# Kernel optimization log

Hardware: AMD Instinct MI355X
Metric: run time of the kernel (lower is better)

Reference implementation:

```python
import jax, jax.numpy as jnp
import numpy as np

INPUT_DIM = 1024
HIDDEN_DIM = 64  # per-head dim
NUM_HEADS = 16
LN_EPS = 1e-5


def setup_inputs() -> dict:
    key = jax.random.key(0)
    ks = jax.random.split(key, 12)
    B, S, D = 2, 2048, INPUT_DIM
    HD = HIDDEN_DIM * NUM_HEADS
    s_in = 1.0 / np.sqrt(D)
    s_hd = 1.0 / np.sqrt(HD)
    return {
        "x": jax.random.normal(ks[0], (B, S, D), dtype=jnp.float32),
        "Wq": jax.random.normal(ks[1], (D, HD), dtype=jnp.float32) * s_in,
        "bq": jax.random.normal(ks[2], (HD,), dtype=jnp.float32) * 0.02,
        "Wk": jax.random.normal(ks[3], (D, HD), dtype=jnp.float32) * s_in,
        "bk": jax.random.normal(ks[4], (HD,), dtype=jnp.float32) * 0.02,
        "Wv": jax.random.normal(ks[5], (D, HD), dtype=jnp.float32) * s_in,
        "bv": jax.random.normal(ks[6], (HD,), dtype=jnp.float32) * 0.02,
        "Wo": jax.random.normal(ks[7], (HD, D), dtype=jnp.float32) * s_hd,
        "bo": jax.random.normal(ks[8], (D,), dtype=jnp.float32) * 0.02,
        "gamma": jnp.ones((D,), dtype=jnp.float32),
        "beta": jnp.zeros((D,), dtype=jnp.float32),
    }


def _layer_norm(y, gamma, beta):
    mu = jnp.mean(y, axis=-1, keepdims=True)
    var = jnp.mean(jnp.square(y - mu), axis=-1, keepdims=True)
    return (y - mu) * jax.lax.rsqrt(var + LN_EPS) * gamma + beta


def reference(x, Wq, bq, Wk, bk, Wv, bv, Wo, bo, gamma, beta):
    B, S, D = x.shape
    H, Hd = NUM_HEADS, HIDDEN_DIM
    # Faithful to the torch module: (B,S,H*Hd) -> reshape (B,H,S,Hd) WITHOUT transpose.
    Q = (x @ Wq + bq).reshape(B, H, S, Hd)
    K = (x @ Wk + bk).reshape(B, H, S, Hd)
    V = (x @ Wv + bv).reshape(B, H, S, Hd)
    scores = jnp.einsum("bhqd,bhkd->bhqk", Q, K) / jnp.sqrt(jnp.float32(Hd))
    attn = jax.nn.softmax(scores, axis=-1)  # dropout=0 -> identity
    ctx = jnp.einsum("bhqk,bhkd->bhqd", attn, V).reshape(B, S, H * Hd)
    out = _layer_norm(x + (ctx @ Wo + bo), gamma, beta)
    return jax.nn.gelu(out, approximate=False)
```

## Files before the change

kernel.cpp:

```cpp
#include <hip/hip_runtime.h>
#include <hip/hip_bf16.h>
#include <cstdint>
#include <cstddef>


#define SEQ   2048
#define DIM   1024
#define NHEAD 16
#define HDIM  64
#define ROWS  4096

#define QSCALE 0.1803368801111204f

typedef __attribute__((ext_vector_type(8))) __bf16 bf16x8;
typedef __attribute__((ext_vector_type(4))) float floatx4;
typedef __attribute__((ext_vector_type(8))) unsigned short ushortx8;

__device__ __forceinline__ unsigned short f2bf(float f) {
  unsigned int u = __float_as_uint(f);
  u += 0x7FFFu + ((u >> 16) & 1u);
  return (unsigned short)(u >> 16);
}

__device__ __forceinline__ unsigned int pk2bf(float a, float b) {
  float2 f; f.x = a; f.y = b;
  __hip_bfloat162 h = __float22bfloat162_rn(f);
  return *(unsigned int*)&h;
}

__device__ __forceinline__ void glds16(const unsigned short* g,
                                       unsigned short* l) {
  __builtin_amdgcn_global_load_lds(
      (const __attribute__((address_space(1))) void*)g,
      (__attribute__((address_space(3))) void*)l, 16, 0, 0);
}

__global__ __launch_bounds__(256) void cvt_bf16(const float* __restrict__ in,
                                                unsigned short* __restrict__ out,
                                                int n4) {
  int i = blockIdx.x * 256 + threadIdx.x;
  if (i >= n4) return;
  float4 v = ((const float4*)in)[i];
  ushort4 o;
  o.x = f2bf(v.x); o.y = f2bf(v.y); o.z = f2bf(v.z); o.w = f2bf(v.w);
  ((ushort4*)out)[i] = o;
}

__global__ __launch_bounds__(256) void transpose_w4(
    const float* __restrict__ Wq, const float* __restrict__ Wk,
    const float* __restrict__ Wv, const float* __restrict__ Wo,
    unsigned short* __restrict__ Wqkvt, unsigned short* __restrict__ Wot) {
  __shared__ float t[32][33];
  const int z = blockIdx.z;
  const float* in = (z == 0) ? Wq : (z == 1) ? Wk : (z == 2) ? Wv : Wo;
  unsigned short* out = (z < 3) ? Wqkvt + (size_t)z * DIM * DIM : Wot;
  const int bx = blockIdx.x * 32, by = blockIdx.y * 32;
  const int tx = threadIdx.x, ty = threadIdx.y;
#pragma unroll
  for (int i = ty; i < 32; i += 8)
    t[i][tx] = in[(size_t)(by + i) * DIM + bx + tx];
  __syncthreads();
#pragma unroll
  for (int i = ty; i < 32; i += 8)
    out[(size_t)(bx + i) * DIM + by + tx] = f2bf(t[tx][i]);
}

__global__ __launch_bounds__(256) void swizzle_kv(
    unsigned short* __restrict__ Kb,
    const unsigned short* __restrict__ Vb,
    unsigned short* __restrict__ Vs) {
  __shared__ unsigned short t[64 * 72];
  const int tile = blockIdx.x;
  const int bh   = blockIdx.y;
  const int isV  = blockIdx.z;
  const int tid  = threadIdx.x;
  const size_t base = (size_t)bh * (SEQ * HDIM) + (size_t)tile * 4096;
  const unsigned short* src = (isV ? Vb : Kb) + base;
#pragma unroll
  for (int p = 0; p < 2; ++p) {
    const int c = p * 256 + tid;
    *(ushortx8*)&t[(c >> 3) * 72 + (c & 7) * 8] = *(const ushortx8*)&src[c * 8];
  }
  __syncthreads();
  unsigned short* dst = (isV ? Vs : Kb) + base;
  const int lane = tid & 63, wave = tid >> 6;
  const int l16 = lane & 15, quad = lane >> 4;
  if (!isV) {
#pragma unroll
    for (int p = 0; p < 2; ++p) {
      const int f = wave * 2 + p;
      const int step = f >> 2, g = f & 3;
      *(ushortx8*)&dst[f * 512 + lane * 8] =
          *(const ushortx8*)&t[(g * 16 + l16) * 72 + step * 32 + quad * 8];
    }
  } else {
#pragma unroll
    for (int p = 0; p < 2; ++p) {
      const int f = wave * 2 + p;
      const int step = f >> 2, g = f & 3;
      ushortx8 v;
#pragma unroll
      for (int e = 0; e < 8; ++e)
        v[e] = t[(step * 32 + quad * 8 + e) * 72 + g * 16 + l16];
      *(ushortx8*)&dst[f * 512 + lane * 8] = v;
    }
  }
}

__global__ __launch_bounds__(256, 3) void gemm_qkv(
    const unsigned short* __restrict__ A,
    const unsigned short* __restrict__ Wt,
    const float* __restrict__ bq, const float* __restrict__ bk,
    const float* __restrict__ bv,
    unsigned short* __restrict__ Qb, unsigned short* __restrict__ Kb,
    unsigned short* __restrict__ Vb) {
  constexpr int K = DIM;
  __shared__ unsigned short As[128 * 64];
  __shared__ unsigned short Bs[128 * 64];
  const int tid  = threadIdx.x;
  const int lane = tid & 63, wave = tid >> 6;
  const int l16  = lane & 15, quad = lane >> 4;
  const int wm   = (wave & 1) * 64, wn = (wave >> 1) * 64;
  const int tm   = blockIdx.y * 128, tn = blockIdx.x * 128;
  const int grow = lane >> 3, gcol = (lane & 7) * 8;

  floatx4 acc[4][4] = {};

  for (int k0 = 0; k0 < K; k0 += 64) {
    __syncthreads();
#pragma unroll
    for (int p = 0; p < 4; ++p) {
      const int q = wave * 4 + p;
      const int row = q * 8 + grow;
      glds16(&A [(size_t)(tm + row) * K + k0 + gcol], &As[q * 512]);
      glds16(&Wt[(size_t)(tn + row) * K + k0 + gcol], &Bs[q * 512]);
    }
    __syncthreads();
#pragma unroll
    for (int step = 0; step < 2; ++step) {
      const int kk = step * 32 + quad * 8;
      bf16x8 af[4], bfr[4];
#pragma unroll
      for (int i = 0; i < 4; ++i)
        af[i] = *(const bf16x8*)&As[(wm + i * 16 + l16) * 64 + kk];
#pragma unroll
      for (int j = 0; j < 4; ++j)
        bfr[j] = *(const bf16x8*)&Bs[(wn + j * 16 + l16) * 64 + kk];
#pragma unroll
      for (int i = 0; i < 4; ++i)
#pragma unroll
        for (int j = 0; j < 4; ++j)
          acc[i][j] = __builtin_amdgcn_mfma_f32_16x16x32_bf16(af[i], bfr[j],
                                                              acc[i][j], 0, 0, 0);
    }
  }

#pragma unroll
  for (int j = 0; j < 4; ++j) {
    const int ng  = tn + wn + j * 16 + l16;
    const int seg = ng >> 10;
    const int col = ng & 1023;
    const float* bp    = (seg == 0) ? bq : (seg == 1) ? bk : bv;
    unsigned short* op = (seg == 0) ? Qb : (seg == 1) ? Kb : Vb;
    const float bias = bp[col];
    const float scl  = (seg == 0) ? QSCALE : 1.0f;
#pragma unroll
    for (int i = 0; i < 4; ++i) {
      const int m0 = tm + wm + i * 16 + quad * 4;
#pragma unroll
      for (int r = 0; r < 4; ++r)
        op[(size_t)(m0 + r) * DIM + col] = f2bf((acc[i][j][r] + bias) * scl);
    }
  }
}

__global__ __launch_bounds__(256) void gemm_o(
    const unsigned short* __restrict__ A,
    const unsigned short* __restrict__ Wt,
    const float* __restrict__ bo,
    float* __restrict__ Y) {
  constexpr int K = DIM;
  __shared__ unsigned short As[128 * 64];
  __shared__ unsigned short Bs[64 * 64];
  const int tid  = threadIdx.x;
  const int lane = tid & 63, wave = tid >> 6;
  const int l16  = lane & 15, quad = lane >> 4;
  const int wm   = wave * 32;
  const int tm   = blockIdx.y * 128, tn = blockIdx.x * 64;
  const int grow = lane >> 3, gcol = (lane & 7) * 8;

  floatx4 acc[2][4] = {};

  for (int k0 = 0; k0 < K; k0 += 64) {
    __syncthreads();
#pragma unroll
    for (int p = 0; p < 4; ++p) {
      const int q = wave * 4 + p;
      const int row = q * 8 + grow;
      glds16(&A[(size_t)(tm + row) * K + k0 + gcol], &As[q * 512]);
    }
#pragma unroll
    for (int p = 0; p < 2; ++p) {
      const int q = wave * 2 + p;
      const int row = q * 8 + grow;
      glds16(&Wt[(size_t)(tn + row) * K + k0 + gcol], &Bs[q * 512]);
    }
    __syncthreads();
#pragma unroll
    for (int step = 0; step < 2; ++step) {
      const int kk = step * 32 + quad * 8;
      bf16x8 af[2], bfr[4];
#pragma unroll
      for (int i = 0; i < 2; ++i)
        af[i] = *(const bf16x8*)&As[(wm + i * 16 + l16) * 64 + kk];
#pragma unroll
      for (int j = 0; j < 4; ++j)
        bfr[j] = *(const bf16x8*)&Bs[(j * 16 + l16) * 64 + kk];
#pragma unroll
      for (int i = 0; i < 2; ++i)
#pragma unroll
        for (int j = 0; j < 4; ++j)
          acc[i][j] = __builtin_amdgcn_mfma_f32_16x16x32_bf16(af[i], bfr[j],
                                                              acc[i][j], 0, 0, 0);
    }
  }

#pragma unroll
  for (int j = 0; j < 4; ++j) {
    const int n = tn + j * 16 + l16;
    const float bias = bo[n];
#pragma unroll
    for (int i = 0; i < 2; ++i) {
      const int m0 = tm + wm + i * 16 + quad * 4;
#pragma unroll
      for (int r = 0; r < 4; ++r)
        Y[(size_t)(m0 + r) * DIM + n] = acc[i][j][r] + bias;
    }
  }
}

__global__ __launch_bounds__(128) void attn_fwd(
    const unsigned short* __restrict__ Qb,
    const unsigned short* __restrict__ Ks,
    const unsigned short* __restrict__ Vs,
    unsigned short* __restrict__ Op0, unsigned short* __restrict__ Op1,
    float* __restrict__ l0, float* __restrict__ l1) {
  __shared__ unsigned short Pl[2][32 * 72];

  const int tid  = threadIdx.x;
  const int lane = tid & 63, wave = tid >> 6;
  const int l16  = lane & 15, quad = lane >> 4;
  const int id   = blockIdx.x;
  const int w    = id >> 3;
  const int head = (id & 7) * 4 + (w & 3);
  const int qt   = (w >> 2) & 31;
  const int half = w >> 7;
  const size_t slab = (size_t)head * SEQ * HDIM;
  const unsigned short* Q  = Qb + slab;
  const unsigned short* Kf = Ks + slab;
  const unsigned short* Vf = Vs + slab;
  const int q0 = qt * 64 + wave * 32;

  bf16x8 qf[2][2];
#pragma unroll
  for (int h = 0; h < 2; ++h) {
    qf[h][0] = *(const bf16x8*)&Q[(size_t)(q0 + h * 16 + l16) * HDIM + quad * 8];
    qf[h][1] = *(const bf16x8*)&Q[(size_t)(q0 + h * 16 + l16) * HDIM + 32 + quad * 8];
  }

  floatx4 o[2][4] = {};
  float lr[2] = {0.f, 0.f};

  for (int t = 0; t < 16; ++t) {
    const int tile = half * 16 + t;
    const unsigned short* kb = Kf + (size_t)tile * 4096;
    const unsigned short* vb = Vf + (size_t)tile * 4096;
    bf16x8 kf[2][4], vf[2][4];
#pragma unroll
    for (int step = 0; step < 2; ++step)
#pragma unroll
      for (int g = 0; g < 4; ++g) {
        kf[step][g] = *(const bf16x8*)&kb[(step * 4 + g) * 512 + lane * 8];
        vf[step][g] = *(const bf16x8*)&vb[(step * 4 + g) * 512 + lane * 8];
      }

    floatx4 s[2][4] = {};
#pragma unroll
    for (int step = 0; step < 2; ++step)
#pragma unroll
      for (int mt = 0; mt < 4; ++mt) {
        s[0][mt] = __builtin_amdgcn_mfma_f32_16x16x32_bf16(kf[step][mt], qf[0][step], s[0][mt], 0, 0, 0);
        s[1][mt] = __builtin_amdgcn_mfma_f32_16x16x32_bf16(kf[step][mt], qf[1][step], s[1][mt], 0, 0, 0);
      }

#pragma unroll
    for (int h = 0; h < 2; ++h) {
#pragma unroll
      for (int mt = 0; mt < 4; ++mt) {
        float p0 = __builtin_amdgcn_exp2f(s[h][mt][0]);
        float p1 = __builtin_amdgcn_exp2f(s[h][mt][1]);
        float p2 = __builtin_amdgcn_exp2f(s[h][mt][2]);
        float p3 = __builtin_amdgcn_exp2f(s[h][mt][3]);
        lr[h] += (p0 + p1) + (p2 + p3);
        uint2 pv;
        pv.x = pk2bf(p0, p1);
        pv.y = pk2bf(p2, p3);
        *(uint2*)&Pl[wave][(h * 16 + l16) * 72 + mt * 16 + quad * 4] = pv;
      }
    }
    __asm__ __volatile__("s_waitcnt lgkmcnt(0)" ::: "memory");

#pragma unroll
    for (int step = 0; step < 2; ++step) {
      const int kk = step * 32 + quad * 8;
      bf16x8 pf0 = *(const bf16x8*)&Pl[wave][(l16) * 72 + kk];
      bf16x8 pf1 = *(const bf16x8*)&Pl[wave][(16 + l16) * 72 + kk];
#pragma unroll
      for (int j = 0; j < 4; ++j) {
        o[0][j] = __builtin_amdgcn_mfma_f32_16x16x32_bf16(pf0, vf[step][j], o[0][j], 0, 0, 0);
        o[1][j] = __builtin_amdgcn_mfma_f32_16x16x32_bf16(pf1, vf[step][j], o[1][j], 0, 0, 0);
      }
    }
  }

#pragma unroll
  for (int h = 0; h < 2; ++h) {
    lr[h] += __shfl_xor(lr[h], 16, 64);
    lr[h] += __shfl_xor(lr[h], 32, 64);
  }
  unsigned short* Op = half ? Op1 : Op0;
  float*          lp = half ? l1 : l0;
#pragma unroll
  for (int h = 0; h < 2; ++h) {
    if (quad == 0)
      lp[head * SEQ + q0 + h * 16 + l16] = lr[h];
#pragma unroll
    for (int j = 0; j < 4; ++j)
#pragma unroll
      for (int r = 0; r < 4; ++r)
        Op[slab + (size_t)(q0 + h * 16 + quad * 4 + r) * HDIM + j * 16 + l16] =
            f2bf(o[h][j][r]);
  }
}

__global__ __launch_bounds__(256) void attn_merge(
    const unsigned short* __restrict__ Op0,
    const unsigned short* __restrict__ Op1,
    const float* __restrict__ l0, const float* __restrict__ l1,
    unsigned short* __restrict__ Cx) {
  const int i = blockIdx.x * 256 + threadIdx.x;
  const float inv = 1.0f / (l0[i >> 3] + l1[i >> 3]);
  ushortx8 a = *(const ushortx8*)&Op0[(size_t)i * 8];
  ushortx8 b = *(const ushortx8*)&Op1[(size_t)i * 8];
  ushortx8 o;
#pragma unroll
  for (int e = 0; e < 8; ++e) {
    const float fa = __uint_as_float((unsigned int)a[e] << 16);
    const float fb = __uint_as_float((unsigned int)b[e] << 16);
    o[e] = f2bf((fa + fb) * inv);
  }
  *(ushortx8*)&Cx[(size_t)i * 8] = o;
}

__global__ __launch_bounds__(256) void ln_gelu(
    const float* __restrict__ x, const float* __restrict__ y,
    const float* __restrict__ gamma, const float* __restrict__ beta,
    float* __restrict__ out) {
  const int row = blockIdx.x;
  const int tid = threadIdx.x;
  const float4 xv = ((const float4*)(x + (size_t)row * DIM))[tid];
  const float4 yv = ((const float4*)(y + (size_t)row * DIM))[tid];
  float4 s;
  s.x = xv.x + yv.x; s.y = xv.y + yv.y; s.z = xv.z + yv.z; s.w = xv.w + yv.w;
  float sum = (s.x + s.y) + (s.z + s.w);
  float sq  = (s.x * s.x + s.y * s.y) + (s.z * s.z + s.w * s.w);
#pragma unroll
  for (int off = 1; off < 64; off <<= 1) {
    sum += __shfl_xor(sum, off, 64);
    sq  += __shfl_xor(sq, off, 64);
  }
  __shared__ float red[8];
  const int wave = tid >> 6, lane = tid & 63;
  if (lane == 0) { red[wave] = sum; red[wave + 4] = sq; }
  __syncthreads();
  sum = red[0] + red[1] + red[2] + red[3];
  sq  = red[4] + red[5] + red[6] + red[7];
  const float mu   = sum * (1.0f / DIM);
  const float var  = sq * (1.0f / DIM) - mu * mu;
  const float rstd = rsqrtf(var + 1e-5f);
  const float4 gv = ((const float4*)gamma)[tid];
  const float4 bv = ((const float4*)beta)[tid];
  float4 ov;
  {
    const float v = (s.x - mu) * rstd * gv.x + bv.x;
    ov.x = 0.5f * v * (1.0f + erff(v * 0.70710678118654752f));
  }
  {
    const float v = (s.y - mu) * rstd * gv.y + bv.y;
    ov.y = 0.5f * v * (1.0f + erff(v * 0.70710678118654752f));
  }
  {
    const float v = (s.z - mu) * rstd * gv.z + bv.z;
    ov.z = 0.5f * v * (1.0f + erff(v * 0.70710678118654752f));
  }
  {
    const float v = (s.w - mu) * rstd * gv.w + bv.w;
    ov.w = 0.5f * v * (1.0f + erff(v * 0.70710678118654752f));
  }
  ((float4*)(out + (size_t)row * DIM))[tid] = ov;
}

extern "C" void kernel_launch(void* const* d_in, const int* in_sizes, int n_in,
                              void* d_out, int out_size, void* d_ws, size_t ws_size,
                              hipStream_t stream) {
  (void)in_sizes; (void)n_in; (void)out_size; (void)ws_size;
  const float* x     = (const float*)d_in[0];
  const float* Wq    = (const float*)d_in[1];
  const float* bq    = (const float*)d_in[2];
  const float* Wk    = (const float*)d_in[3];
  const float* bk    = (const float*)d_in[4];
  const float* Wv    = (const float*)d_in[5];
  const float* bv    = (const float*)d_in[6];
  const float* Wo    = (const float*)d_in[7];
  const float* bo    = (const float*)d_in[8];
  const float* gamma = (const float*)d_in[9];
  const float* beta  = (const float*)d_in[10];
  float* out = (float*)d_out;

  char* ws = (char*)d_ws;
  const size_t MB = 1u << 20;
  unsigned short* xb    = (unsigned short*)(ws);
  unsigned short* Op0   = (unsigned short*)(ws);
  unsigned short* Wqkvt = (unsigned short*)(ws + 8 * MB);
  float*          lp0   = (float*)(ws + 8 * MB);
  float*          lp1   = (float*)(ws + 8 * MB + 256 * 1024);
  unsigned short* Wot   = (unsigned short*)(ws + 14 * MB);
  unsigned short* Qb    = (unsigned short*)(ws + 16 * MB);
  unsigned short* Kb    = (unsigned short*)(ws + 24 * MB);
  unsigned short* Vs    = (unsigned short*)(ws + 32 * MB);
  unsigned short* Vb    = (unsigned short*)(ws + 40 * MB);
  unsigned short* Cx    = (unsigned short*)(ws + 40 * MB);
  float*          Y     = (float*)(ws + 48 * MB);
  unsigned short* Op1   = (unsigned short*)(ws + 48 * MB);

  cvt_bf16<<<(ROWS * DIM / 4 + 255) / 256, 256, 0, stream>>>(x, xb, ROWS * DIM / 4);
  transpose_w4<<<dim3(32, 32, 4), dim3(32, 8), 0, stream>>>(Wq, Wk, Wv, Wo, Wqkvt, Wot);

  gemm_qkv<<<dim3(24, 32), 256, 0, stream>>>(xb, Wqkvt, bq, bk, bv, Qb, Kb, Vb);
  swizzle_kv<<<dim3(SEQ / 64, 32, 2), 256, 0, stream>>>(Kb, Vb, Vs);
  attn_fwd<<<2048, 128, 0, stream>>>(Qb, Kb, Vs, Op0, Op1, lp0, lp1);
  attn_merge<<<(ROWS * DIM) / (8 * 256), 256, 0, stream>>>(Op0, Op1, lp0, lp1, Cx);
  gemm_o<<<dim3(16, 32), 256, 0, stream>>>(Cx, Wot, bo, Y);
  ln_gelu<<<ROWS, 256, 0, stream>>>(x, Y, gamma, beta, out);
}
```

Baseline: 220.4 us.

## Fuse split-K attention merge into attn_fwd via LDS and merge prep kernels

```diff
diff --git a/kernel.cpp b/kernel.cpp
--- a/kernel.cpp
+++ b/kernel.cpp
@@ -35,27 +35,31 @@
       (__attribute__((address_space(3))) void*)l, 16, 0, 0);
 }
 
-__global__ __launch_bounds__(256) void cvt_bf16(const float* __restrict__ in,
-                                                unsigned short* __restrict__ out,
-                                                int n4) {
-  int i = blockIdx.x * 256 + threadIdx.x;
-  if (i >= n4) return;
-  float4 v = ((const float4*)in)[i];
-  ushort4 o;
-  o.x = f2bf(v.x); o.y = f2bf(v.y); o.z = f2bf(v.z); o.w = f2bf(v.w);
-  ((ushort4*)out)[i] = o;
-}
-
-__global__ __launch_bounds__(256) void transpose_w4(
+__global__ __launch_bounds__(256) void prep_all(
+    const float* __restrict__ x,
     const float* __restrict__ Wq, const float* __restrict__ Wk,
     const float* __restrict__ Wv, const float* __restrict__ Wo,
+    unsigned short* __restrict__ xb,
     unsigned short* __restrict__ Wqkvt, unsigned short* __restrict__ Wot) {
   __shared__ float t[32][33];
   const int z = blockIdx.z;
+  const int tx = threadIdx.x, ty = threadIdx.y;
+  if (z == 4) {
+    const int bid = blockIdx.y * 32 + blockIdx.x;
+    const int tid = ty * 32 + tx;
+#pragma unroll
+    for (int p = 0; p < 4; ++p) {
+      const int i = bid * 1024 + p * 256 + tid;
+      float4 v = ((const float4*)x)[i];
+      ushort4 o;
+      o.x = f2bf(v.x); o.y = f2bf(v.y); o.z = f2bf(v.z); o.w = f2bf(v.w);
+      ((ushort4*)xb)[i] = o;
+    }
+    return;
+  }
   const float* in = (z == 0) ? Wq : (z == 1) ? Wk : (z == 2) ? Wv : Wo;
   unsigned short* out = (z < 3) ? Wqkvt + (size_t)z * DIM * DIM : Wot;
   const int bx = blockIdx.x * 32, by = blockIdx.y * 32;
-  const int tx = threadIdx.x, ty = threadIdx.y;
 #pragma unroll
   for (int i = ty; i < 32; i += 8)
     t[i][tx] = in[(size_t)(by + i) * DIM + bx + tx];
@@ -239,13 +243,12 @@
   }
 }
 
-__global__ __launch_bounds__(128) void attn_fwd(
+__global__ __launch_bounds__(256) void attn_fwd(
     const unsigned short* __restrict__ Qb,
     const unsigned short* __restrict__ Ks,
     const unsigned short* __restrict__ Vs,
-    unsigned short* __restrict__ Op0, unsigned short* __restrict__ Op1,
-    float* __restrict__ l0, float* __restrict__ l1) {
-  __shared__ unsigned short Pl[2][32 * 72];
+    unsigned short* __restrict__ ctx) {
+  __shared__ unsigned short Pl[4][32 * 72];
 
   const int tid  = threadIdx.x;
   const int lane = tid & 63, wave = tid >> 6;
@@ -253,13 +256,12 @@
   const int id   = blockIdx.x;
   const int w    = id >> 3;
   const int head = (id & 7) * 4 + (w & 3);
-  const int qt   = (w >> 2) & 31;
-  const int half = w >> 7;
+  const int qt   = w >> 2;
   const size_t slab = (size_t)head * SEQ * HDIM;
   const unsigned short* Q  = Qb + slab;
   const unsigned short* Kf = Ks + slab;
   const unsigned short* Vf = Vs + slab;
-  const int q0 = qt * 64 + wave * 32;
+  const int q0 = qt * 32;
 
   bf16x8 qf[2][2];
 #pragma unroll
@@ -271,8 +273,8 @@
   floatx4 o[2][4] = {};
   float lr[2] = {0.f, 0.f};
 
-  for (int t = 0; t < 16; ++t) {
-    const int tile = half * 16 + t;
+  for (int t = 0; t < 8; ++t) {
+    const int tile = wave * 8 + t;
     const unsigned short* kb = Kf + (size_t)tile * 4096;
     const unsigned short* vb = Vf + (size_t)tile * 4096;
     bf16x8 kf[2][4], vf[2][4];
@@ -328,38 +330,48 @@
     lr[h] += __shfl_xor(lr[h], 16, 64);
     lr[h] += __shfl_xor(lr[h], 32, 64);
   }
-  unsigned short* Op = half ? Op1 : Op0;
-  float*          lp = half ? l1 : l0;
-#pragma unroll
-  for (int h = 0; h < 2; ++h) {
-    if (quad == 0)
-      lp[head * SEQ + q0 + h * 16 + l16] = lr[h];
-#pragma unroll
-    for (int j = 0; j < 4; ++j)
+
+  if (wave != 0) {
+#pragma unroll
+    for (int h = 0; h < 2; ++h) {
+      if (quad == 0)
+        *(float*)&Pl[wave][2048 + 2 * (h * 16 + l16)] = lr[h];
+#pragma unroll
+      for (int j = 0; j < 4; ++j)
+#pragma unroll
+        for (int r = 0; r < 4; ++r)
+          Pl[wave][(h * 16 + quad * 4 + r) * 64 + j * 16 + l16] =
+              f2bf(o[h][j][r]);
+    }
+  }
+  __syncthreads();
+
+  if (wave == 0) {
+    unsigned short* cp = ctx + slab;
+#pragma unroll
+    for (int h = 0; h < 2; ++h) {
+      float lt = lr[h];
+#pragma unroll
+      for (int p = 1; p < 4; ++p)
+        lt += *(const float*)&Pl[p][2048 + 2 * (h * 16 + l16)];
+      float lb[4];
 #pragma unroll
       for (int r = 0; r < 4; ++r)
-        Op[slab + (size_t)(q0 + h * 16 + quad * 4 + r) * HDIM + j * 16 + l16] =
-            f2bf(o[h][j][r]);
-  }
-}
-
-__global__ __launch_bounds__(256) void attn_merge(
-    const unsigned short* __restrict__ Op0,
-    const unsigned short* __restrict__ Op1,
-    const float* __restrict__ l0, const float* __restrict__ l1,
-    unsigned short* __restrict__ Cx) {
-  const int i = blockIdx.x * 256 + threadIdx.x;
-  const float inv = 1.0f / (l0[i >> 3] + l1[i >> 3]);
-  ushortx8 a = *(const ushortx8*)&Op0[(size_t)i * 8];
-  ushortx8 b = *(const ushortx8*)&Op1[(size_t)i * 8];
-  ushortx8 o;
-#pragma unroll
-  for (int e = 0; e < 8; ++e) {
-    const float fa = __uint_as_float((unsigned int)a[e] << 16);
-    const float fb = __uint_as_float((unsigned int)b[e] << 16);
-    o[e] = f2bf((fa + fb) * inv);
-  }
-  *(ushortx8*)&Cx[(size_t)i * 8] = o;
+        lb[r] = 1.0f / __shfl(lt, quad * 4 + r, 64);
+#pragma unroll
+      for (int j = 0; j < 4; ++j)
+#pragma unroll
+        for (int r = 0; r < 4; ++r) {
+          const int row = h * 16 + quad * 4 + r;
+          float v = o[h][j][r];
+#pragma unroll
+          for (int p = 1; p < 4; ++p)
+            v += __uint_as_float(
+                (unsigned int)Pl[p][row * 64 + j * 16 + l16] << 16);
+          cp[(size_t)(q0 + row) * HDIM + j * 16 + l16] = f2bf(v * lb[r]);
+        }
+    }
+  }
 }
 
 __global__ __launch_bounds__(256) void ln_gelu(
@@ -430,10 +442,7 @@
   char* ws = (char*)d_ws;
   const size_t MB = 1u << 20;
   unsigned short* xb    = (unsigned short*)(ws);
-  unsigned short* Op0   = (unsigned short*)(ws);
   unsigned short* Wqkvt = (unsigned short*)(ws + 8 * MB);
-  float*          lp0   = (float*)(ws + 8 * MB);
-  float*          lp1   = (float*)(ws + 8 * MB + 256 * 1024);
   unsigned short* Wot   = (unsigned short*)(ws + 14 * MB);
   unsigned short* Qb    = (unsigned short*)(ws + 16 * MB);
   unsigned short* Kb    = (unsigned short*)(ws + 24 * MB);
@@ -441,15 +450,12 @@
   unsigned short* Vb    = (unsigned short*)(ws + 40 * MB);
   unsigned short* Cx    = (unsigned short*)(ws + 40 * MB);
   float*          Y     = (float*)(ws + 48 * MB);
-  unsigned short* Op1   = (unsigned short*)(ws + 48 * MB);
-
-  cvt_bf16<<<(ROWS * DIM / 4 + 255) / 256, 256, 0, stream>>>(x, xb, ROWS * DIM / 4);
-  transpose_w4<<<dim3(32, 32, 4), dim3(32, 8), 0, stream>>>(Wq, Wk, Wv, Wo, Wqkvt, Wot);
-
+
+  prep_all<<<dim3(32, 32, 5), dim3(32, 8), 0, stream>>>(x, Wq, Wk, Wv, Wo,
+                                                        xb, Wqkvt, Wot);
   gemm_qkv<<<dim3(24, 32), 256, 0, stream>>>(xb, Wqkvt, bq, bk, bv, Qb, Kb, Vb);
   swizzle_kv<<<dim3(SEQ / 64, 32, 2), 256, 0, stream>>>(Kb, Vb, Vs);
-  attn_fwd<<<2048, 128, 0, stream>>>(Qb, Kb, Vs, Op0, Op1, lp0, lp1);
-  attn_merge<<<(ROWS * DIM) / (8 * 256), 256, 0, stream>>>(Op0, Op1, lp0, lp1, Cx);
+  attn_fwd<<<2048, 256, 0, stream>>>(Qb, Kb, Vs, Cx);
   gemm_o<<<dim3(16, 32), 256, 0, stream>>>(Cx, Wot, bo, Y);
   ln_gelu<<<ROWS, 256, 0, stream>>>(x, Y, gamma, beta, out);
 }
```

After: 218.6 us. No clear change (-0.8%).
